# Kernel optimization log

Measured on AMD Instinct MI355X. Metric: run time of the kernel, lower is better.

## Reference

```python
import jax, jax.numpy as jnp
import numpy as np

B, TE, TD, D = 8, 2048, 2048, 256

def setup_inputs() -> dict:
    key = jax.random.key(0)
    k1, k2 = jax.random.split(key)
    encoder_outputs = jax.random.normal(k1, (B, TE, D), dtype=jnp.float32)
    decoder_outputs = jax.random.normal(k2, (B, TD, D), dtype=jnp.float32)
    return {"encoder_outputs": encoder_outputs, "decoder_outputs": decoder_outputs}

def reference(encoder_outputs, decoder_outputs):
    # luong_score[b,e,t] = sum_d enc[b,e,d] * dec[b,t,d]   (batch_dot with dec transposed)
    luong_score = jnp.einsum('bed,btd->bet', encoder_outputs, decoder_outputs)
    # softmax over encoder-time axis (axis=1)
    luong_score = jax.nn.softmax(luong_score, axis=1)
    # original does expand_dims + broadcast-multiply + sum over axis=1;
    # same math as a contraction over e: context[b,t,d] = sum_e score[b,e,t]*enc[b,e,d]
    encoder_vector = jnp.einsum('bet,bed->btd', luong_score, encoder_outputs)
    return jnp.concatenate([decoder_outputs, encoder_vector], axis=-1)
```

## Files before the change

kernel.cpp:

```cpp
#include <hip/hip_runtime.h>

typedef _Float16 f16;
typedef _Float16 f16x4 __attribute__((ext_vector_type(4)));
typedef _Float16 f16x8 __attribute__((ext_vector_type(8)));
typedef float    f32x4 __attribute__((ext_vector_type(4)));

#define NB   8
#define TE   2048
#define TD   2048
#define DIM  256
#define NSPLIT 2
#define LOG2E 1.44269504088896340736f

#define AS1(p) ((const __attribute__((address_space(1))) void*)(p))
#define AS3(p) ((__attribute__((address_space(3))) void*)(p))

__global__ __launch_bounds__(256) void prep_kernel(const float* __restrict__ enc,
                                                   f16* __restrict__ ench,
                                                   f16* __restrict__ enct) {
    __shared__ f16 tile[64][72];
    int b  = blockIdx.z;
    int e0 = blockIdx.x * 64;
    int d0 = blockIdx.y * 64;
    int tid = threadIdx.x;
    {
        int e  = tid >> 2;
        int dg = (tid & 3) * 16;
        const float* p = enc + ((size_t)b * TE + e0 + e) * DIM + d0 + dg;
        float4 v0 = *(const float4*)(p);
        float4 v1 = *(const float4*)(p + 4);
        float4 v2 = *(const float4*)(p + 8);
        float4 v3 = *(const float4*)(p + 12);
        f16x8 o0, o1;
        o0[0]=(f16)v0.x; o0[1]=(f16)v0.y; o0[2]=(f16)v0.z; o0[3]=(f16)v0.w;
        o0[4]=(f16)v1.x; o0[5]=(f16)v1.y; o0[6]=(f16)v1.z; o0[7]=(f16)v1.w;
        o1[0]=(f16)v2.x; o1[1]=(f16)v2.y; o1[2]=(f16)v2.z; o1[3]=(f16)v2.w;
        o1[4]=(f16)v3.x; o1[5]=(f16)v3.y; o1[6]=(f16)v3.z; o1[7]=(f16)v3.w;
        *(f16x8*)&tile[e][dg]     = o0;
        *(f16x8*)&tile[e][dg + 8] = o1;
        f16* hp = ench + ((size_t)b * TE + e0 + e) * DIM + d0 + dg;
        *(f16x8*)(hp)     = o0;
        *(f16x8*)(hp + 8) = o1;
    }
    __syncthreads();
    {
        int d  = tid >> 2;
        int eg = (tid & 3) * 16;
        f16x8 o0, o1;
        #pragma unroll
        for (int ii = 0; ii < 8; ii++) o0[ii] = tile[eg + ii][d];
        #pragma unroll
        for (int ii = 0; ii < 8; ii++) o1[ii] = tile[eg + 8 + ii][d];
        f16* qp = enct + ((size_t)b * DIM + d0 + d) * TE + e0 + eg;
        *(f16x8*)(qp)     = o0;
        *(f16x8*)(qp + 8) = o1;
    }
}

#define LDS_NAT0 0
#define LDS_NAT1 16384
#define LDS_TR0  32768
#define LDS_TR1  49152
#define LDS_P    65536

__global__ __launch_bounds__(256, 2) void attn_kernel(
        const float* __restrict__ dec32,
        const f16*  __restrict__ enc_h,
        const f16*  __restrict__ enc_t,
        float* __restrict__ out,
        f16*   __restrict__ ctxp,
        float* __restrict__ m_arr,
        float* __restrict__ l_arr,
        int nsplit) {
    __shared__ char lds[75776];
    const int tid  = threadIdx.x;
    const int lane = tid & 63;
    const int wave = tid >> 6;
    const int th   = wave >> 1;
    const int dh   = wave & 1;
    const int tcol = lane & 15;
    const int q    = lane >> 4;

    int xb, b, z, iters, e_base;
    if (nsplit == NSPLIT) {
        int fid = blockIdx.x + 32 * (blockIdx.y + 8 * blockIdx.z);
        int c = fid & 7, j = fid >> 3;
        xb = j & 31;
        int g = c * 2 + (j >> 5);
        b = g & 7; z = g >> 3;
        iters  = 32;
        e_base = z * 1024;
    } else { xb = blockIdx.x; b = blockIdx.y; z = 0; iters = 64; e_base = 0; }
    const int  t0    = xb * 64;
    const bool heavy = (dh == (xb & 1));

    const f16* enc_b  = enc_h + (size_t)b * TE * DIM;
    const f16* enct_b = enc_t + (size_t)b * DIM * TE;

    const int e00 = tid >> 5, cs0 = tid & 31;
    const int nat_g0 = e00 * DIM + (cs0 ^ (e00 & 7)) * 8;
    const int d00 = tid >> 2, c00 = tid & 3;
    const int tr_g0  = d00 * TE + (c00 ^ ((d00 >> 1) & 3)) * 8;
    const int l0     = wave * 1024;

    #pragma unroll
    for (int i = 0; i < 4; i++)
        __builtin_amdgcn_global_load_lds(AS1(enc_b + (size_t)e_base * DIM + nat_g0 + i * 2048),
                                         AS3(lds + LDS_NAT0 + l0 + i * 4096), 16, 0, 0);
    #pragma unroll
    for (int i = 0; i < 4; i++)
        __builtin_amdgcn_global_load_lds(AS1(enc_b + (size_t)(e_base + 32) * DIM + nat_g0 + i * 2048),
                                         AS3(lds + LDS_NAT1 + l0 + i * 4096), 16, 0, 0);
    #pragma unroll
    for (int i = 0; i < 4; i++)
        __builtin_amdgcn_global_load_lds(AS1(enct_b + e_base + tr_g0 + i * 64 * TE),
                                         AS3(lds + LDS_TR0 + l0 + i * 4096), 16, 0, 0);

    if (nsplit == 1) {
        const float* dp = dec32 + ((size_t)b * TD + t0) * DIM;
        float*       op = out   + ((size_t)b * TD + t0) * 512;
        #pragma unroll
        for (int i = 0; i < 16; i++) {
            int idx = i * 256 + tid;
            int t = idx >> 6, c = idx & 63;
            float4 v = *(const float4*)(dp + t * DIM + c * 4);
            *(float4*)(op + t * 512 + c * 4) = v;
        }
    }

    f16x8 qf[2][8];
    if (heavy) {
        const float* qp = dec32 + ((size_t)b * TD + t0 + th * 32) * DIM;
        #pragma unroll
        for (int tn = 0; tn < 2; tn++)
            #pragma unroll
            for (int ks = 0; ks < 8; ks++) {
                const float* p = qp + (size_t)(tn * 16 + tcol) * DIM + ks * 32 + q * 8;
                float4 u = *(const float4*)(p);
                float4 v = *(const float4*)(p + 4);
                f16x8 o;
                o[0]=(f16)u.x; o[1]=(f16)u.y; o[2]=(f16)u.z; o[3]=(f16)u.w;
                o[4]=(f16)v.x; o[5]=(f16)v.y; o[6]=(f16)v.z; o[7]=(f16)v.w;
                qf[tn][ks] = o;
            }
    }

    f16x8 ones;
    #pragma unroll
    for (int j = 0; j < 8; j++) ones[j] = (f16)1.0f;

    const f32x4 zero4 = {0.f, 0.f, 0.f, 0.f};
    float m_[2] = {-INFINITY, -INFINITY};
    f32x4 lsum[2] = {zero4, zero4};
    f32x4 ctx[8][2];
    #pragma unroll
    for (int dm = 0; dm < 8; dm++)
        #pragma unroll
        for (int tn = 0; tn < 2; tn++) ctx[dm][tn] = zero4;

    const int e7 = tcol & 7;

    __syncthreads();

    for (int it = 0; it < iters; it++) {
        const int natc = (it & 1) ? LDS_NAT1 : LDS_NAT0;
        const int trc  = (it & 1) ? LDS_TR1  : LDS_TR0;
        char* pb = lds + LDS_P + ((it & 1) ? 5120 : 0) + th * 2560;

        if (heavy) {
            f32x4 st[2][2];
            #pragma unroll
            for (int mt = 0; mt < 2; mt++)
                #pragma unroll
                for (int tn = 0; tn < 2; tn++) st[mt][tn] = zero4;
            #pragma unroll
            for (int ks = 0; ks < 8; ks++) {
                #pragma unroll
                for (int mt = 0; mt < 2; mt++) {
                    int e = mt * 16 + tcol;
                    f16x8 af = *(const f16x8*)(lds + natc + e * 512 + (((ks << 2) | q) ^ e7) * 16);
                    #pragma unroll
                    for (int tn = 0; tn < 2; tn++)
                        st[mt][tn] = __builtin_amdgcn_mfma_f32_16x16x32_f16(af, qf[tn][ks], st[mt][tn], 0, 0, 0);
                }
            }
            #pragma unroll
            for (int tn = 0; tn < 2; tn++) {
                float mx = fmaxf(fmaxf(fmaxf(st[0][tn][0], st[0][tn][1]), fmaxf(st[0][tn][2], st[0][tn][3])),
                                 fmaxf(fmaxf(st[1][tn][0], st[1][tn][1]), fmaxf(st[1][tn][2], st[1][tn][3])));
                mx = fmaxf(mx, __shfl_xor(mx, 16, 64));
                mx = fmaxf(mx, __shfl_xor(mx, 32, 64));
                float mn = fmaxf(m_[tn], mx);
                bool bumped = mn > m_[tn];
                float al = __builtin_amdgcn_exp2f((m_[tn] - mn) * LOG2E);
                m_[tn] = mn;
                char* prow = pb + (tn * 16 + tcol) * 80;
                #pragma unroll
                for (int mt = 0; mt < 2; mt++) {
                    f16x4 pv;
                    #pragma unroll
                    for (int r = 0; r < 4; r++)
                        pv[r] = (f16)__builtin_amdgcn_exp2f((st[mt][tn][r] - mn) * LOG2E);
                    *(f16x4*)(prow + mt * 32 + q * 8) = pv;
                }
                if (q == 0) *(float*)(prow + 72) = al;
                if (__any(bumped)) {
                    lsum[tn][0] *= al; lsum[tn][1] *= al; lsum[tn][2] *= al; lsum[tn][3] *= al;
                    #pragma unroll
                    for (int dm = 0; dm < 8; dm++) {
                        ctx[dm][tn][0] *= al; ctx[dm][tn][1] *= al;
                        ctx[dm][tn][2] *= al; ctx[dm][tn][3] *= al;
                    }
                }
            }
        }

        __syncthreads();

        if (it + 1 < iters) {
            const int trn = (it & 1) ? LDS_TR0 : LDS_TR1;
            const int e1  = e_base + (it + 1) * 32;
            #pragma unroll
            for (int i = 0; i < 4; i++)
                __builtin_amdgcn_global_load_lds(AS1(enct_b + e1 + tr_g0 + i * 64 * TE),
                                                 AS3(lds + trn + l0 + i * 4096), 16, 0, 0);
        }
        if (it + 2 < iters) {
            const int e2 = e_base + (it + 2) * 32;
            #pragma unroll
            for (int i = 0; i < 4; i++)
                __builtin_amdgcn_global_load_lds(AS1(enc_b + (size_t)e2 * DIM + nat_g0 + i * 2048),
                                                 AS3(lds + natc + l0 + i * 4096), 16, 0, 0);
        }

        if (!heavy) {
            #pragma unroll
            for (int tn = 0; tn < 2; tn++) {
                float al = *(const float*)(pb + (tn * 16 + tcol) * 80 + 72);
                if (__any(al < 1.0f)) {
                    lsum[tn][0] *= al; lsum[tn][1] *= al; lsum[tn][2] *= al; lsum[tn][3] *= al;
                    #pragma unroll
                    for (int dm = 0; dm < 8; dm++) {
                        ctx[dm][tn][0] *= al; ctx[dm][tn][1] *= al;
                        ctx[dm][tn][2] *= al; ctx[dm][tn][3] *= al;
                    }
                }
            }
        }

        f16x8 pf[2];
        #pragma unroll
        for (int tn = 0; tn < 2; tn++)
            pf[tn] = *(const f16x8*)(pb + (tn * 16 + tcol) * 80 + q * 16);
        #pragma unroll
        for (int tn = 0; tn < 2; tn++)
            lsum[tn] = __builtin_amdgcn_mfma_f32_16x16x32_f16(ones, pf[tn], lsum[tn], 0, 0, 0);
        #pragma unroll
        for (int dm = 0; dm < 8; dm++) {
            int drow = dh * 128 + dm * 16 + tcol;
            f16x8 af = *(const f16x8*)(lds + trc + drow * 64 + (q ^ ((tcol >> 1) & 3)) * 16);
            #pragma unroll
            for (int tn = 0; tn < 2; tn++)
                ctx[dm][tn] = __builtin_amdgcn_mfma_f32_16x16x32_f16(af, pf[tn], ctx[dm][tn], 0, 0, 0);
        }
    }

    if (nsplit > 1) {
        size_t rowbase = (size_t)(z * NB + b) * TD + t0 + th * 32;
        #pragma unroll
        for (int tn = 0; tn < 2; tn++) {
            float inv = 1.0f / lsum[tn][0];
            size_t rb = (rowbase + tn * 16 + tcol) * DIM + dh * 128;
            #pragma unroll
            for (int dm = 0; dm < 8; dm++) {
                f16x4 cv;
                #pragma unroll
                for (int r = 0; r < 4; r++) cv[r] = (f16)(ctx[dm][tn][r] * inv);
                *(f16x4*)(ctxp + rb + dm * 16 + q * 4) = cv;
            }
        }
        if (heavy && lane < 16) {
            int mi = (z * NB + b) * TD + t0 + th * 32 + lane;
            #pragma unroll
            for (int tn = 0; tn < 2; tn++) {
                m_arr[mi + tn * 16] = m_[tn];
                l_arr[mi + tn * 16] = lsum[tn][0];
            }
        }
    } else {
        float* ob = out + ((size_t)b * TD + t0 + th * 32) * 512 + 256 + dh * 128;
        #pragma unroll
        for (int tn = 0; tn < 2; tn++) {
            float inv = 1.0f / lsum[tn][0];
            #pragma unroll
            for (int dm = 0; dm < 8; dm++)
                #pragma unroll
                for (int r = 0; r < 4; r++)
                    ob[(size_t)(tn * 16 + tcol) * 512 + dm * 16 + q * 4 + r] = ctx[dm][tn][r] * inv;
        }
    }
}

__global__ __launch_bounds__(256) void combine_kernel(const float* __restrict__ dec32,
        const f16* __restrict__ ctxp, const float* __restrict__ m_arr,
        const float* __restrict__ l_arr, float* __restrict__ out) {
    int idx  = blockIdx.x * 256 + threadIdx.x;
    int trow = idx >> 5;
    int dg   = (idx & 31) * 8;
    float m0[NSPLIT], l0[NSPLIT], M = -INFINITY;
    #pragma unroll
    for (int s = 0; s < NSPLIT; s++) {
        m0[s] = m_arr[s * (NB * TD) + trow];
        l0[s] = l_arr[s * (NB * TD) + trow];
        M = fmaxf(M, m0[s]);
    }
    float L = 0.f, w[NSPLIT];
    #pragma unroll
    for (int s = 0; s < NSPLIT; s++) {
        w[s] = __builtin_amdgcn_exp2f((m0[s] - M) * LOG2E) * l0[s];
        L += w[s];
    }
    float invL = 1.0f / L;
    float acc[8] = {0.f,0.f,0.f,0.f,0.f,0.f,0.f,0.f};
    #pragma unroll
    for (int s = 0; s < NSPLIT; s++) {
        f16x8 v = *(const f16x8*)(ctxp + ((size_t)s * (NB * TD) + trow) * DIM + dg);
        float ws = w[s] * invL;
        #pragma unroll
        for (int j = 0; j < 8; j++) acc[j] += ws * (float)v[j];
    }
    float4 d0 = *(const float4*)(dec32 + (size_t)trow * DIM + dg);
    float4 d1 = *(const float4*)(dec32 + (size_t)trow * DIM + dg + 4);
    float* ob = out + (size_t)trow * 512;
    *(float4*)(ob + dg)     = d0;
    *(float4*)(ob + dg + 4) = d1;
    float4 c0, c1;
    c0.x=acc[0]; c0.y=acc[1]; c0.z=acc[2]; c0.w=acc[3];
    c1.x=acc[4]; c1.y=acc[5]; c1.z=acc[6]; c1.w=acc[7];
    *(float4*)(ob + 256 + dg)     = c0;
    *(float4*)(ob + 256 + dg + 4) = c1;
}

extern "C" void kernel_launch(void* const* d_in, const int* in_sizes, int n_in,
                              void* d_out, int out_size, void* d_ws, size_t ws_size,
                              hipStream_t stream) {
    (void)in_sizes; (void)n_in;
    const float* enc = (const float*)d_in[0];
    const float* dec = (const float*)d_in[1];
    float* out = (float*)d_out;

    const size_t HB    = (size_t)NB * TE * DIM * 2;
    const size_t CTXPB = (size_t)NSPLIT * NB * TD * DIM * 2;
    const size_t MLB   = (size_t)NSPLIT * NB * TD * 4;
    const size_t NEED2 = 2 * HB + CTXPB + 2 * MLB;
    const size_t NEED1 = 2 * HB;

    if (ws_size < NEED1) {
        hipMemsetAsync(d_out, 0, (size_t)out_size * sizeof(float), stream);
        return;
    }
    int nsplit = (ws_size >= NEED2) ? NSPLIT : 1;

    f16*   enc_h = (f16*)d_ws;
    f16*   enc_t = (f16*)((char*)d_ws + HB);
    f16*   ctxp  = (f16*)((char*)d_ws + 2 * HB);
    float* m_arr = (float*)((char*)d_ws + 2 * HB + CTXPB);
    float* l_arr = (float*)((char*)d_ws + 2 * HB + CTXPB + MLB);

    prep_kernel<<<dim3(32, 4, 8), 256, 0, stream>>>(enc, enc_h, enc_t);
    attn_kernel<<<dim3(32, 8, nsplit), 256, 0, stream>>>(dec, enc_h, enc_t, out,
                                                         ctxp, m_arr, l_arr, nsplit);
    if (nsplit == NSPLIT)
        combine_kernel<<<2048, 256, 0, stream>>>(dec, ctxp, m_arr, l_arr, out);
}
```

Before: 152.0 us.

## Split score computation across both wave halves and move decoder copy into attn kernel

Previously only the "heavy" waves computed QK^T scores and softmax for both 16-row t tiles, while the other waves idled and only rescaled. Now every wave computes scores for its own 16-row tile, selected by dh, so the MFMA and exp work is balanced across waves and each wave keeps fewer query fragments in registers. Each wave reads the other wave's alpha from LDS to rescale its context accumulators. Separately, the decoder passthrough copy moves from the combine kernel into the z==0 split of the attn kernel, so combine only writes the context half.

Result: slower. 516.3 us (+239.7%).

```diff
diff --git a/kernel.cpp b/kernel.cpp
--- a/kernel.cpp
+++ b/kernel.cpp
@@ -91,8 +91,7 @@
         iters  = 32;
         e_base = z * 1024;
     } else { xb = blockIdx.x; b = blockIdx.y; z = 0; iters = 64; e_base = 0; }
-    const int  t0    = xb * 64;
-    const bool heavy = (dh == (xb & 1));
+    const int t0 = xb * 64;
 
     const f16* enc_b  = enc_h + (size_t)b * TE * DIM;
     const f16* enct_b = enc_t + (size_t)b * DIM * TE;
@@ -116,7 +115,7 @@
         __builtin_amdgcn_global_load_lds(AS1(enct_b + e_base + tr_g0 + i * 64 * TE),
                                          AS3(lds + LDS_TR0 + l0 + i * 4096), 16, 0, 0);
 
-    if (nsplit == 1) {
+    if (nsplit == 1 || z == 0) {
         const float* dp = dec32 + ((size_t)b * TD + t0) * DIM;
         float*       op = out   + ((size_t)b * TD + t0) * 512;
         #pragma unroll
@@ -128,21 +127,19 @@
         }
     }
 
-    f16x8 qf[2][8];
-    if (heavy) {
-        const float* qp = dec32 + ((size_t)b * TD + t0 + th * 32) * DIM;
-        #pragma unroll
-        for (int tn = 0; tn < 2; tn++)
-            #pragma unroll
-            for (int ks = 0; ks < 8; ks++) {
-                const float* p = qp + (size_t)(tn * 16 + tcol) * DIM + ks * 32 + q * 8;
-                float4 u = *(const float4*)(p);
-                float4 v = *(const float4*)(p + 4);
-                f16x8 o;
-                o[0]=(f16)u.x; o[1]=(f16)u.y; o[2]=(f16)u.z; o[3]=(f16)u.w;
-                o[4]=(f16)v.x; o[5]=(f16)v.y; o[6]=(f16)v.z; o[7]=(f16)v.w;
-                qf[tn][ks] = o;
-            }
+    f16x8 qf[8];
+    {
+        const float* qp = dec32 + ((size_t)b * TD + t0 + th * 32 + dh * 16 + tcol) * DIM;
+        #pragma unroll
+        for (int ks = 0; ks < 8; ks++) {
+            const float* p = qp + ks * 32 + q * 8;
+            float4 u = *(const float4*)(p);
+            float4 v = *(const float4*)(p + 4);
+            f16x8 o;
+            o[0]=(f16)u.x; o[1]=(f16)u.y; o[2]=(f16)u.z; o[3]=(f16)u.w;
+            o[4]=(f16)v.x; o[5]=(f16)v.y; o[6]=(f16)v.z; o[7]=(f16)v.w;
+            qf[ks] = o;
+        }
     }
 
     f16x8 ones;
@@ -150,7 +147,7 @@
     for (int j = 0; j < 8; j++) ones[j] = (f16)1.0f;
 
     const f32x4 zero4 = {0.f, 0.f, 0.f, 0.f};
-    float m_[2] = {-INFINITY, -INFINITY};
+    float m_ = -INFINITY;
     f32x4 lsum[2] = {zero4, zero4};
     f32x4 ctx[8][2];
     #pragma unroll
@@ -167,50 +164,44 @@
         const int trc  = (it & 1) ? LDS_TR1  : LDS_TR0;
         char* pb = lds + LDS_P + ((it & 1) ? 5120 : 0) + th * 2560;
 
-        if (heavy) {
-            f32x4 st[2][2];
-            #pragma unroll
-            for (int mt = 0; mt < 2; mt++)
-                #pragma unroll
-                for (int tn = 0; tn < 2; tn++) st[mt][tn] = zero4;
-            #pragma unroll
-            for (int ks = 0; ks < 8; ks++) {
-                #pragma unroll
-                for (int mt = 0; mt < 2; mt++) {
-                    int e = mt * 16 + tcol;
-                    f16x8 af = *(const f16x8*)(lds + natc + e * 512 + (((ks << 2) | q) ^ e7) * 16);
-                    #pragma unroll
-                    for (int tn = 0; tn < 2; tn++)
-                        st[mt][tn] = __builtin_amdgcn_mfma_f32_16x16x32_f16(af, qf[tn][ks], st[mt][tn], 0, 0, 0);
-                }
-            }
-            #pragma unroll
-            for (int tn = 0; tn < 2; tn++) {
-                float mx = fmaxf(fmaxf(fmaxf(st[0][tn][0], st[0][tn][1]), fmaxf(st[0][tn][2], st[0][tn][3])),
-                                 fmaxf(fmaxf(st[1][tn][0], st[1][tn][1]), fmaxf(st[1][tn][2], st[1][tn][3])));
-                mx = fmaxf(mx, __shfl_xor(mx, 16, 64));
-                mx = fmaxf(mx, __shfl_xor(mx, 32, 64));
-                float mn = fmaxf(m_[tn], mx);
-                bool bumped = mn > m_[tn];
-                float al = __builtin_amdgcn_exp2f((m_[tn] - mn) * LOG2E);
-                m_[tn] = mn;
-                char* prow = pb + (tn * 16 + tcol) * 80;
-                #pragma unroll
-                for (int mt = 0; mt < 2; mt++) {
-                    f16x4 pv;
-                    #pragma unroll
-                    for (int r = 0; r < 4; r++)
-                        pv[r] = (f16)__builtin_amdgcn_exp2f((st[mt][tn][r] - mn) * LOG2E);
-                    *(f16x4*)(prow + mt * 32 + q * 8) = pv;
-                }
-                if (q == 0) *(float*)(prow + 72) = al;
-                if (__any(bumped)) {
-                    lsum[tn][0] *= al; lsum[tn][1] *= al; lsum[tn][2] *= al; lsum[tn][3] *= al;
-                    #pragma unroll
-                    for (int dm = 0; dm < 8; dm++) {
-                        ctx[dm][tn][0] *= al; ctx[dm][tn][1] *= al;
-                        ctx[dm][tn][2] *= al; ctx[dm][tn][3] *= al;
-                    }
+        f32x4 st[2];
+        st[0] = zero4; st[1] = zero4;
+        #pragma unroll
+        for (int ks = 0; ks < 8; ks++) {
+            #pragma unroll
+            for (int mt = 0; mt < 2; mt++) {
+                int e = mt * 16 + tcol;
+                f16x8 af = *(const f16x8*)(lds + natc + e * 512 + (((ks << 2) | q) ^ e7) * 16);
+                st[mt] = __builtin_amdgcn_mfma_f32_16x16x32_f16(af, qf[ks], st[mt], 0, 0, 0);
+            }
+        }
+
+        float al;
+        {
+            float mx = fmaxf(fmaxf(fmaxf(st[0][0], st[0][1]), fmaxf(st[0][2], st[0][3])),
+                             fmaxf(fmaxf(st[1][0], st[1][1]), fmaxf(st[1][2], st[1][3])));
+            mx = fmaxf(mx, __shfl_xor(mx, 16, 64));
+            mx = fmaxf(mx, __shfl_xor(mx, 32, 64));
+            float mn = fmaxf(m_, mx);
+            bool bumped = mn > m_;
+            al = __builtin_amdgcn_exp2f((m_ - mn) * LOG2E);
+            m_ = mn;
+            char* prow = pb + (dh * 16 + tcol) * 80;
+            #pragma unroll
+            for (int mt = 0; mt < 2; mt++) {
+                f16x4 pv;
+                #pragma unroll
+                for (int r = 0; r < 4; r++)
+                    pv[r] = (f16)__builtin_amdgcn_exp2f((st[mt][r] - mn) * LOG2E);
+                *(f16x4*)(prow + mt * 32 + q * 8) = pv;
+            }
+            if (q == 0) *(float*)(prow + 72) = al;
+            if (__any(bumped)) {
+                lsum[dh][0] *= al; lsum[dh][1] *= al; lsum[dh][2] *= al; lsum[dh][3] *= al;
+                #pragma unroll
+                for (int dm = 0; dm < 8; dm++) {
+                    ctx[dm][dh][0] *= al; ctx[dm][dh][1] *= al;
+                    ctx[dm][dh][2] *= al; ctx[dm][dh][3] *= al;
                 }
             }
         }
@@ -233,17 +224,15 @@
                                                  AS3(lds + natc + l0 + i * 4096), 16, 0, 0);
         }
 
-        if (!heavy) {
-            #pragma unroll
-            for (int tn = 0; tn < 2; tn++) {
-                float al = *(const float*)(pb + (tn * 16 + tcol) * 80 + 72);
-                if (__any(al < 1.0f)) {
-                    lsum[tn][0] *= al; lsum[tn][1] *= al; lsum[tn][2] *= al; lsum[tn][3] *= al;
-                    #pragma unroll
-                    for (int dm = 0; dm < 8; dm++) {
-                        ctx[dm][tn][0] *= al; ctx[dm][tn][1] *= al;
-                        ctx[dm][tn][2] *= al; ctx[dm][tn][3] *= al;
-                    }
+        {
+            int ot = dh ^ 1;
+            float al2 = *(const float*)(pb + (ot * 16 + tcol) * 80 + 72);
+            if (__any(al2 < 1.0f)) {
+                lsum[ot][0] *= al2; lsum[ot][1] *= al2; lsum[ot][2] *= al2; lsum[ot][3] *= al2;
+                #pragma unroll
+                for (int dm = 0; dm < 8; dm++) {
+                    ctx[dm][ot][0] *= al2; ctx[dm][ot][1] *= al2;
+                    ctx[dm][ot][2] *= al2; ctx[dm][ot][3] *= al2;
                 }
             }
         }
@@ -279,12 +268,11 @@
                 *(f16x4*)(ctxp + rb + dm * 16 + q * 4) = cv;
             }
         }
-        if (heavy && lane < 16) {
-            int mi = (z * NB + b) * TD + t0 + th * 32 + lane;
-            #pragma unroll
-            for (int tn = 0; tn < 2; tn++) {
-                m_arr[mi + tn * 16] = m_[tn];
-                l_arr[mi + tn * 16] = lsum[tn][0];
+        if (lane < 16) {
+            int mi = (int)((z * NB + b) * TD) + t0 + th * 32 + dh * 16 + lane;
+            if (wave < 2 || 1) {
+                m_arr[mi] = m_;
+                l_arr[mi] = lsum[dh][0];
             }
         }
     } else {
@@ -301,7 +289,7 @@
     }
 }
 
-__global__ __launch_bounds__(256) void combine_kernel(const float* __restrict__ dec32,
+__global__ __launch_bounds__(256) void combine_kernel(
         const f16* __restrict__ ctxp, const float* __restrict__ m_arr,
         const float* __restrict__ l_arr, float* __restrict__ out) {
     int idx  = blockIdx.x * 256 + threadIdx.x;
@@ -329,16 +317,12 @@
         #pragma unroll
         for (int j = 0; j < 8; j++) acc[j] += ws * (float)v[j];
     }
-    float4 d0 = *(const float4*)(dec32 + (size_t)trow * DIM + dg);
-    float4 d1 = *(const float4*)(dec32 + (size_t)trow * DIM + dg + 4);
-    float* ob = out + (size_t)trow * 512;
-    *(float4*)(ob + dg)     = d0;
-    *(float4*)(ob + dg + 4) = d1;
+    float* ob = out + (size_t)trow * 512 + 256;
     float4 c0, c1;
     c0.x=acc[0]; c0.y=acc[1]; c0.z=acc[2]; c0.w=acc[3];
     c1.x=acc[4]; c1.y=acc[5]; c1.z=acc[6]; c1.w=acc[7];
-    *(float4*)(ob + 256 + dg)     = c0;
-    *(float4*)(ob + 256 + dg + 4) = c1;
+    *(float4*)(ob + dg)     = c0;
+    *(float4*)(ob + dg + 4) = c1;
 }
 
 extern "C" void kernel_launch(void* const* d_in, const int* in_sizes, int n_in,
@@ -371,5 +355,5 @@
     attn_kernel<<<dim3(32, 8, nsplit), 256, 0, stream>>>(dec, enc_h, enc_t, out,
                                                          ctxp, m_arr, l_arr, nsplit);
     if (nsplit == NSPLIT)
-        combine_kernel<<<2048, 256, 0, stream>>>(dec, ctxp, m_arr, l_arr, out);
+        combine_kernel<<<2048, 256, 0, stream>>>(ctxp, m_arr, l_arr, out);
 }
```
